# Kernel optimization log

Measured on AMD Instinct MI355X. Metric: run time of the kernel, lower is better.

## Reference

```python
import jax, jax.numpy as jnp
import numpy as np

EMBED = 768
NHEADS = 12
HEAD_DIM = EMBED // NHEADS
LA_HEADS = 16
MLP_HID = EMBED * 4
EPS = 1e-5


def setup_inputs() -> dict:
    key = jax.random.key(0)
    ks = jax.random.split(key, 16)
    s = lambda fan_in: 1.0 / np.sqrt(fan_in)
    inp = {
        "x": jax.random.normal(ks[0], (64, 197, EMBED), dtype=jnp.float32),
        "norm1_g": jnp.ones((EMBED,), jnp.float32),
        "norm1_b": jnp.zeros((EMBED,), jnp.float32),
        "qkv_w": jax.random.normal(ks[1], (3 * EMBED, EMBED), jnp.float32) * s(EMBED),
        "qkv_b": jnp.zeros((3 * EMBED,), jnp.float32),
        "proj_w": jax.random.normal(ks[2], (EMBED, EMBED), jnp.float32) * s(EMBED),
        "proj_b": jnp.zeros((EMBED,), jnp.float32),
        "norm2_g": jnp.ones((EMBED,), jnp.float32),
        "norm2_b": jnp.zeros((EMBED,), jnp.float32),
        "fc1_w": jax.random.normal(ks[3], (MLP_HID, EMBED), jnp.float32) * s(EMBED),
        "fc1_b": jnp.zeros((MLP_HID,), jnp.float32),
        "fc2_w": jax.random.normal(ks[4], (EMBED, MLP_HID), jnp.float32) * s(MLP_HID),
        "fc2_b": jnp.zeros((EMBED,), jnp.float32),
        # LA params: f1 Conv2d(16,1,1) -> weight [16]; f2 Conv2d(1,16,1) -> weight [16]; v Conv2d(2,1,1) -> weight [2]
        "f1_w": jax.random.normal(ks[5], (LA_HEADS,), jnp.float32) * s(LA_HEADS),
        "f1_b": jnp.zeros((1,), jnp.float32),
        "f2_w": jax.random.normal(ks[6], (LA_HEADS,), jnp.float32),
        "f2_b": jnp.zeros((LA_HEADS,), jnp.float32),
        "v_w": jax.random.normal(ks[7], (2,), jnp.float32) * s(2),
        "v_b": jnp.zeros((1,), jnp.float32),
    }
    return inp


def _layernorm(x, g, b):
    mu = x.mean(-1, keepdims=True)
    var = jnp.mean((x - mu) ** 2, -1, keepdims=True)
    return (x - mu) * jax.lax.rsqrt(var + EPS) * g + b


def _la(x, f1_w, f1_b, f2_w, f2_b, v_w, v_b):
    # x: [B, C=768, 14, 14]; 16 channel groups of 48, pooled over 7x7 grid of 2x2 patches
    B, C, H, W = x.shape
    g = C // LA_HEADS
    xr = x.reshape(B, LA_HEADS, g, 7, 2, 7, 2)
    means = xr.mean(axis=(2, 4, 6))            # [B,16,7,7]
    maxs = xr.max(axis=(2, 4, 6))              # [B,16,7,7]

    def channel_mlp(t):  # f2(relu(f1(t))), 1x1 convs across the 16 "head" channels
        h = jnp.einsum('bchw,c->bhw', t, f1_w) + f1_b[0]
        h = jax.nn.relu(h)
        return h[:, None, :, :] * f2_w[None, :, None, None] + f2_b[None, :, None, None]

    m = channel_mlp(means)
    mx = channel_mlp(maxs)
    fusion = v_w[0] * m + v_w[1] * mx + v_b[0]   # [B,16,7,7]
    # bilinear upsample 7x7 -> 14x14, align_corners=False (half-pixel centers)
    fusion = jax.image.resize(fusion, (B, LA_HEADS, 14, 14), method='bilinear')
    gate = jax.nn.sigmoid(fusion)                # [B,16,14,14]
    out = x.reshape(B, LA_HEADS, g, H, W) * gate[:, :, None, :, :]
    return out.reshape(B, C, H, W) + x


def _attn(x, qkv_w, qkv_b, proj_w, proj_b):
    B, N, D = x.shape
    qkv = x @ qkv_w.T + qkv_b
    qkv = qkv.reshape(B, N, 3, NHEADS, HEAD_DIM).transpose(2, 0, 3, 1, 4)
    q, k, v = qkv[0], qkv[1], qkv[2]             # [B,H,N,hd]
    scores = jnp.einsum('bhnd,bhmd->bhnm', q, k) * (HEAD_DIM ** -0.5)
    a = jax.nn.softmax(scores, axis=-1)
    o = jnp.einsum('bhnm,bhmd->bhnd', a, v)
    o = o.transpose(0, 2, 1, 3).reshape(B, N, D)
    return o @ proj_w.T + proj_b


def reference(x, norm1_g, norm1_b, qkv_w, qkv_b, proj_w, proj_b,
              norm2_g, norm2_b, fc1_w, fc1_b, fc2_w, fc2_b,
              f1_w, f1_b, f2_w, f2_b, v_w, v_b):
    B, N, C = x.shape
    cls_tok = x[:, :1, :]                        # [B,1,C]
    spatial = x[:, 1:, :]                        # [B,196,C]
    H = W = 14
    x_la = spatial.reshape(B, H, W, C).transpose(0, 3, 1, 2)   # [B,C,14,14]
    x_la = _la(x_la, f1_w, f1_b, f2_w, f2_b, v_w, v_b)
    x_la = x_la.reshape(B, C, H * W).transpose(0, 2, 1)        # [B,196,C]
    x_cat = jnp.concatenate([cls_tok, x_la], axis=1)           # [B,197,C]
    x = x + _attn(_layernorm(x_cat, norm1_g, norm1_b), qkv_w, qkv_b, proj_w, proj_b)
    h = _layernorm(x, norm2_g, norm2_b)
    h = jax.nn.gelu(h @ fc1_w.T + fc1_b, approximate=False)
    x = x + (h @ fc2_w.T + fc2_b)
    return x
```

## Files before the change

kernel.cpp:

```cpp
#include <hip/hip_runtime.h>
#include <hip/hip_bf16.h>
#include <math.h>

using bf16 = __hip_bfloat16;
using short8 = __attribute__((ext_vector_type(8))) short;
using floatx4 = __attribute__((ext_vector_type(4))) float;

constexpr int B = 64;
constexpr int N = 197;
constexpr int C = 768;
constexpr int NH = 12;
constexpr int HD = 64;
constexpr int HID = 3072;
constexpr int M = B * N;
constexpr int MPAD = 12672;
constexpr int MT = MPAD / 128;
constexpr int MTP = 104;
constexpr float EPS = 1e-5f;

__device__ __forceinline__ float b2f(bf16 v) { return __bfloat162float(v); }
__device__ __forceinline__ bf16 f2b(float v) { return __float2bfloat16(v); }

typedef const __attribute__((address_space(1))) unsigned int* gas1_t;
typedef __attribute__((address_space(3))) unsigned int* las3_t;
__device__ __forceinline__ void load_lds16(const bf16* g, bf16* l) {
  __builtin_amdgcn_global_load_lds((gas1_t)g, (las3_t)l, 16, 0, 0);
}

__global__ void cvt_wf_kernel(const float* __restrict__ src, bf16* __restrict__ dst,
                              int Nc, int K) {
  int i = blockIdx.x * 256 + threadIdx.x;
  int total = Nc * (K >> 3);
  if (i >= total) return;
  int k8 = i % (K >> 3);
  int n  = i / (K >> 3);
  int kc = k8 >> 2, quad = k8 & 3;
  int nb = n >> 7, nn = n & 127, tp = nn >> 4, l = nn & 15;
  int KC = K >> 5;
  size_t di = (((size_t)nb * KC + kc) * 8 + tp) * 512 + quad * 128 + l * 8;
  const float* s = src + (size_t)n * K + k8 * 8;
  #pragma unroll
  for (int e = 0; e < 8; ++e) dst[di + e] = f2b(s[e]);
}

__device__ __forceinline__ float block_sum(float v, float* red) {
  #pragma unroll
  for (int off = 32; off >= 1; off >>= 1) v += __shfl_xor(v, off, 64);
  int w = threadIdx.x >> 6;
  if ((threadIdx.x & 63) == 0) red[w] = v;
  __syncthreads();
  float r = red[0] + red[1] + red[2] + red[3];
  __syncthreads();
  return r;
}

__global__ void la_pool_kernel(const float* __restrict__ x,
                               const float* __restrict__ f1w, const float* __restrict__ f1bias,
                               const float* __restrict__ f2w, const float* __restrict__ f2bias,
                               const float* __restrict__ vw,  const float* __restrict__ vbias,
                               float* __restrict__ fusion7) {
  int blk = blockIdx.x;
  int b = blk / 49, p = blk % 49;
  int h7 = p / 7, w7 = p % 7;
  int tid = threadIdx.x;
  int head = tid >> 4;
  int j = tid & 15;

  float sum = 0.f, mx = -3.0e38f;
  #pragma unroll
  for (int a = 0; a < 2; ++a) {
    #pragma unroll
    for (int bb = 0; bb < 2; ++bb) {
      int tok = 1 + (2 * h7 + a) * 14 + (2 * w7 + bb);
      const float* row = x + ((size_t)b * N + tok) * C + head * 48;
      #pragma unroll
      for (int s = 0; s < 3; ++s) {
        float v = row[j + 16 * s];
        sum += v;
        mx = fmaxf(mx, v);
      }
    }
  }
  #pragma unroll
  for (int off = 8; off >= 1; off >>= 1) {
    sum += __shfl_xor(sum, off, 64);
    mx = fmaxf(mx, __shfl_xor(mx, off, 64));
  }
  __shared__ float s_mean[16], s_max[16];
  if (j == 0) { s_mean[head] = sum / 192.f; s_max[head] = mx; }
  __syncthreads();
  if (tid < 16) {
    float hm = f1bias[0], hx = hm;
    #pragma unroll
    for (int h = 0; h < 16; ++h) {
      float w = f1w[h];
      hm += s_mean[h] * w;
      hx += s_max[h] * w;
    }
    hm = fmaxf(hm, 0.f);
    hx = fmaxf(hx, 0.f);
    float w2 = f2w[tid], b2v = f2bias[tid];
    float m   = hm * w2 + b2v;
    float mxv = hx * w2 + b2v;
    float fus = vw[0] * m + vw[1] * mxv + vbias[0];
    fusion7[((size_t)b * 16 + tid) * 49 + p] = fus;
  }
}

__global__ void gate_ln1_kernel(const float* __restrict__ x, const float* __restrict__ fusion7,
                                const float* __restrict__ g, const float* __restrict__ beta,
                                bf16* __restrict__ ln1) {
  int blk = blockIdx.x;
  int b = blk / N, n = blk % N;
  int tid = threadIdx.x;
  __shared__ float gates[16];
  __shared__ float red[4];

  if (tid < 16) {
    if (n > 0) {
      int hh = (n - 1) / 14, ww = (n - 1) % 14;
      float ch = fminf(fmaxf(hh * 0.5f - 0.25f, 0.f), 6.f);
      float cw = fminf(fmaxf(ww * 0.5f - 0.25f, 0.f), 6.f);
      int h0 = (int)floorf(ch); int h1 = min(h0 + 1, 6); float fh = ch - (float)h0;
      int w0 = (int)floorf(cw); int w1 = min(w0 + 1, 6); float fw = cw - (float)w0;
      const float* fp = fusion7 + ((size_t)b * 16 + tid) * 49;
      float v00 = fp[h0 * 7 + w0], v01 = fp[h0 * 7 + w1];
      float v10 = fp[h1 * 7 + w0], v11 = fp[h1 * 7 + w1];
      float v = (1.f - fh) * ((1.f - fw) * v00 + fw * v01)
              + fh        * ((1.f - fw) * v10 + fw * v11);
      gates[tid] = 1.f / (1.f + expf(-v));
    } else {
      gates[tid] = 0.f;
    }
  }
  __syncthreads();

  const float* xr = x + ((size_t)b * N + n) * C;
  float v[3];
  #pragma unroll
  for (int s = 0; s < 3; ++s) {
    int c = tid + 256 * s;
    v[s] = xr[c] * (1.f + gates[c / 48]);
  }
  float mu = block_sum(v[0] + v[1] + v[2], red) * (1.f / 768.f);
  float d0 = v[0] - mu, d1 = v[1] - mu, d2 = v[2] - mu;
  float var = block_sum(d0 * d0 + d1 * d1 + d2 * d2, red) * (1.f / 768.f);
  float rs = rsqrtf(var + EPS);
  bf16* orow = ln1 + ((size_t)b * N + n) * C;
  #pragma unroll
  for (int s = 0; s < 3; ++s) {
    int c = tid + 256 * s;
    orow[c] = f2b((v[s] - mu) * rs * g[c] + beta[c]);
  }
}

__global__ void ln_bf16_kernel(const bf16* __restrict__ xin,
                               const float* __restrict__ g, const float* __restrict__ beta,
                               bf16* __restrict__ out) {
  int row = blockIdx.x;
  int tid = threadIdx.x;
  __shared__ float red[4];
  const bf16* xr = xin + (size_t)row * C;
  float v[3];
  #pragma unroll
  for (int s = 0; s < 3; ++s) v[s] = b2f(xr[tid + 256 * s]);
  float mu = block_sum(v[0] + v[1] + v[2], red) * (1.f / 768.f);
  float d0 = v[0] - mu, d1 = v[1] - mu, d2 = v[2] - mu;
  float var = block_sum(d0 * d0 + d1 * d1 + d2 * d2, red) * (1.f / 768.f);
  float rs = rsqrtf(var + EPS);
  bf16* orow = out + (size_t)row * C;
  #pragma unroll
  for (int s = 0; s < 3; ++s) {
    int c = tid + 256 * s;
    orow[c] = f2b((v[s] - mu) * rs * g[c] + beta[c]);
  }
}

template <int EPI, int K>
__global__ void __launch_bounds__(256, 3)
gemm128(const bf16* __restrict__ A, const bf16* __restrict__ Wf,
        const float* __restrict__ bias,
        const float* __restrict__ resF, const bf16* __restrict__ resB,
        bf16* __restrict__ outB, float* __restrict__ outF, int Nc) {
  constexpr int KC = K >> 5;
  static_assert(KC % 3 == 0, "KC must be divisible by 3 for the unroll");
  constexpr int CW = (K == 768) ? 6 : 3;
  constexpr int PERCH = 13 * CW;
  int nx = Nc >> 7;
  int g = blockIdx.x;
  int c = g & 7;
  int t = g >> 3;
  int ch = t / PERCH;
  int r  = t % PERCH;
  int j  = r / CW;
  int x  = ch * CW + (r % CW);
  int y  = c + 8 * j;
  if (y >= MT) return;
  int m0 = y * 128;
  int n0 = x * 128;

  __shared__ __align__(16) char smem[49152];
  bf16* sA = (bf16*)smem;
  bf16* sB = (bf16*)(smem + 24576);

  int tid = threadIdx.x;
  int wave = tid >> 6, lane = tid & 63, quad = lane >> 4, l16 = lane & 15;

  int ln16 = lane >> 2, seg = lane & 3;
  int sw = seg ^ ((ln16 >> 1) & 3);
  const bf16* gA = A + (size_t)(m0 + wave * 32 + ln16) * K + sw * 8;

  const bf16* gB = Wf + ((size_t)(n0 >> 7) * KC) * 4096 + (size_t)(wave * 2) * 512 + lane * 8;

  int wm = (wave & 1) * 64, wn = (wave >> 1) * 64;
  int csw = (l16 >> 1) & 3;
  int tp0 = wn >> 4;

  floatx4 acc[4][4] = {};

  bf16* dA0 = sA + (wave * 32) * 32;
  bf16* dB0 = sB + (wave * 2) * 512;

  auto stageTo = [&](const bf16* gAs, const bf16* gBs, int bufOff) {
    load_lds16(gAs, dA0 + bufOff);
    load_lds16(gAs + (size_t)16 * K, dA0 + bufOff + 16 * 32);
    load_lds16(gBs, dB0 + bufOff);
    load_lds16(gBs + 512, dB0 + bufOff + 512);
  };

  stageTo(gA, gB, 0);
  stageTo(gA + 32, gB + 4096, 4096);

  const bf16* gAs = gA + 64;
  const bf16* gBs = gB + 8192;

  const bf16* aRd = sA + (wm + l16) * 32 + (quad ^ csw) * 8;
  const bf16* bRd = sB + tp0 * 512 + lane * 8;

  auto body = [&](int bufOff, int stageBufOff, bool doStage, bool lastIter) {
    if (lastIter) {
      asm volatile("s_waitcnt vmcnt(0) lgkmcnt(0)" ::: "memory");
    } else {
      asm volatile("s_waitcnt vmcnt(4) lgkmcnt(0)" ::: "memory");
    }
    __builtin_amdgcn_s_barrier();
    __builtin_amdgcn_sched_barrier(0);

    short8 bw[4];
    #pragma unroll
    for (int t2 = 0; t2 < 4; ++t2)
      bw[t2] = *reinterpret_cast<const short8*>(bRd + bufOff + t2 * 512);
    short8 af[4];
    #pragma unroll
    for (int s = 0; s < 4; ++s)
      af[s] = *reinterpret_cast<const short8*>(aRd + bufOff + s * 16 * 32);

    if (doStage) {
      stageTo(gAs, gBs, stageBufOff);
      gAs += 32;
      gBs += 4096;
    }

    __builtin_amdgcn_s_setprio(1);
    #pragma unroll
    for (int s = 0; s < 4; ++s)
      #pragma unroll
      for (int t2 = 0; t2 < 4; ++t2)
        acc[s][t2] = __builtin_amdgcn_mfma_f32_16x16x32_bf16(af[s], bw[t2], acc[s][t2], 0, 0, 0);
    __builtin_amdgcn_s_setprio(0);
  };

  for (int kc0 = 0; kc0 < KC; kc0 += 3) {
    bool lastGrp = (kc0 + 3 >= KC);
    body(0,    8192, true,      false);
    body(4096, 0,    !lastGrp,  false);
    body(8192, 4096, !lastGrp,  lastGrp);
  }

  if (!resF && !resB && outB) {
    __syncthreads();
    bf16* sC = (bf16*)smem;
    constexpr int SCS = 136;
    #pragma unroll
    for (int t2 = 0; t2 < 4; ++t2) {
      int col = wn + t2 * 16 + l16;
      float bv = bias[n0 + col];
      #pragma unroll
      for (int s = 0; s < 4; ++s) {
        int rowb = wm + s * 16 + quad * 4;
        #pragma unroll
        for (int r2 = 0; r2 < 4; ++r2) {
          float v = acc[s][t2][r2] + bv;
          if (EPI == 1) v = 0.5f * v * (1.f + erff(v * 0.7071067811865475f));
          sC[(rowb + r2) * SCS + col] = f2b(v);
        }
      }
    }
    __syncthreads();
    int rl = tid >> 4, cl = tid & 15;
    #pragma unroll
    for (int i = 0; i < 8; ++i) {
      int row = i * 16 + rl;
      int gr = m0 + row;
      if (gr < M) {
        short8 vv = *reinterpret_cast<const short8*>(sC + row * SCS + cl * 8);
        *reinterpret_cast<short8*>(outB + (size_t)gr * Nc + n0 + cl * 8) = vv;
      }
    }
  } else {
    #pragma unroll
    for (int t2 = 0; t2 < 4; ++t2) {
      int col = n0 + wn + t2 * 16 + l16;
      float bv = bias[col];
      #pragma unroll
      for (int s = 0; s < 4; ++s) {
        int rowb = m0 + wm + s * 16 + quad * 4;
        #pragma unroll
        for (int r2 = 0; r2 < 4; ++r2) {
          int row = rowb + r2;
          if (row < M) {
            float v = acc[s][t2][r2] + bv;
            if (EPI == 1) v = 0.5f * v * (1.f + erff(v * 0.7071067811865475f));
            size_t idx = (size_t)row * Nc + col;
            if (resF) v += resF[idx];
            if (resB) v += b2f(resB[idx]);
            if (outF) outF[idx] = v;
            if (outB) outB[idx] = f2b(v);
          }
        }
      }
    }
  }
}

__global__ void __launch_bounds__(256, 2)
attn_mfma_kernel(const bf16* __restrict__ qkv, bf16* __restrict__ attn_o) {
  int bh = blockIdx.x;
  int h = bh % NH, b = bh / NH;
  int tid = threadIdx.x;
  int wave = tid >> 6, lane = tid & 63, quad = lane >> 4, l16 = lane & 15;

  __shared__ __align__(16) bf16 sVt[64][232];
  __shared__ __align__(16) bf16 sP[4][16][232];

  const bf16* base = qkv + (size_t)b * N * 2304 + h * 64;

  {
    int d = tid & 63;
    for (int m = tid >> 6; m < 224; m += 4) {
      sVt[d][m] = (m < N) ? base[(size_t)m * 2304 + 1536 + d] : f2b(0.f);
    }
  }
  __syncthreads();

  const float scale = 0.125f;

  for (int qt = wave; qt < 13; qt += 4) {
    int qr = min(qt * 16 + l16, N - 1);
    const bf16* qp = base + (size_t)qr * 2304;
    short8 aq0 = *reinterpret_cast<const short8*>(qp + quad * 8);
    short8 aq1 = *reinterpret_cast<const short8*>(qp + 32 + quad * 8);

    floatx4 s[13];
    short8 bk0c, bk1c;
    {
      int kr = min(l16, N - 1);
      const bf16* kp = base + (size_t)kr * 2304 + 768;
      bk0c = *reinterpret_cast<const short8*>(kp + quad * 8);
      bk1c = *reinterpret_cast<const short8*>(kp + 32 + quad * 8);
    }
    #pragma unroll
    for (int kt = 0; kt < 13; ++kt) {
      short8 bk0n, bk1n;
      if (kt < 12) {
        int kr = min((kt + 1) * 16 + l16, N - 1);
        const bf16* kp = base + (size_t)kr * 2304 + 768;
        bk0n = *reinterpret_cast<const short8*>(kp + quad * 8);
        bk1n = *reinterpret_cast<const short8*>(kp + 32 + quad * 8);
      }
      floatx4 acc = floatx4{0.f, 0.f, 0.f, 0.f};
      acc = __builtin_amdgcn_mfma_f32_16x16x32_bf16(aq0, bk0c, acc, 0, 0, 0);
      acc = __builtin_amdgcn_mfma_f32_16x16x32_bf16(aq1, bk1c, acc, 0, 0, 0);
      s[kt] = acc;
      if (kt < 12) { bk0c = bk0n; bk1c = bk1n; }
    }

    bool cv[13];
    #pragma unroll
    for (int kt = 0; kt < 13; ++kt) cv[kt] = (kt * 16 + l16) < N;

    float mx[4] = {-3.0e38f, -3.0e38f, -3.0e38f, -3.0e38f};
    #pragma unroll
    for (int kt = 0; kt < 13; ++kt) {
      #pragma unroll
      for (int r = 0; r < 4; ++r) {
        float sv = s[kt][r] * scale;
        s[kt][r] = sv;
        if (cv[kt]) mx[r] = fmaxf(mx[r], sv);
      }
    }
    #pragma unroll
    for (int off = 8; off >= 1; off >>= 1) {
      #pragma unroll
      for (int r = 0; r < 4; ++r) mx[r] = fmaxf(mx[r], __shfl_xor(mx[r], off, 64));
    }
    float sum[4] = {0.f, 0.f, 0.f, 0.f};
    #pragma unroll
    for (int kt = 0; kt < 13; ++kt) {
      #pragma unroll
      for (int r = 0; r < 4; ++r) {
        float e = cv[kt] ? __expf(s[kt][r] - mx[r]) : 0.f;
        s[kt][r] = e;
        sum[r] += e;
      }
    }
    #pragma unroll
    for (int off = 8; off >= 1; off >>= 1) {
      #pragma unroll
      for (int r = 0; r < 4; ++r) sum[r] += __shfl_xor(sum[r], off, 64);
    }
    float inv[4];
    #pragma unroll
    for (int r = 0; r < 4; ++r) inv[r] = 1.f / sum[r];

    #pragma unroll
    for (int kt = 0; kt < 13; ++kt) {
      #pragma unroll
      for (int r = 0; r < 4; ++r)
        sP[wave][quad * 4 + r][kt * 16 + l16] = f2b(s[kt][r]);
    }
    #pragma unroll
    for (int r = 0; r < 4; ++r)
      sP[wave][quad * 4 + r][208 + l16] = f2b(0.f);

    floatx4 o[4] = {floatx4{0,0,0,0}, floatx4{0,0,0,0}, floatx4{0,0,0,0}, floatx4{0,0,0,0}};
    #pragma unroll
    for (int c = 0; c < 7; ++c) {
      short8 ap = *reinterpret_cast<const short8*>(&sP[wave][l16][c * 32 + quad * 8]);
      #pragma unroll
      for (int t = 0; t < 4; ++t) {
        short8 bv = *reinterpret_cast<const short8*>(&sVt[t * 16 + l16][c * 32 + quad * 8]);
        o[t] = __builtin_amdgcn_mfma_f32_16x16x32_bf16(ap, bv, o[t], 0, 0, 0);
      }
    }

    asm volatile("s_waitcnt lgkmcnt(0)" ::: "memory");
    bf16* sO = &sP[wave][0][0];
    constexpr int SOS = 72;
    #pragma unroll
    for (int t = 0; t < 4; ++t) {
      #pragma unroll
      for (int r = 0; r < 4; ++r)
        sO[(quad * 4 + r) * SOS + t * 16 + l16] = f2b(o[t][r] * inv[r]);
    }
    asm volatile("s_waitcnt lgkmcnt(0)" ::: "memory");
    int orow = lane >> 3, ocol = (lane & 7) * 8;
    #pragma unroll
    for (int i = 0; i < 2; ++i) {
      int row = i * 8 + orow;
      int qrow = qt * 16 + row;
      if (qrow < N) {
        short8 vv = *reinterpret_cast<const short8*>(sO + row * SOS + ocol);
        *reinterpret_cast<short8*>(attn_o + ((size_t)b * N + qrow) * C + h * 64 + ocol) = vv;
      }
    }
    asm volatile("s_waitcnt lgkmcnt(0)" ::: "memory");
  }
}

extern "C" void kernel_launch(void* const* d_in, const int* in_sizes, int n_in,
                              void* d_out, int out_size, void* d_ws, size_t ws_size,
                              hipStream_t stream) {
  (void)in_sizes; (void)n_in; (void)out_size; (void)ws_size;
  const float* x       = (const float*)d_in[0];
  const float* norm1_g = (const float*)d_in[1];
  const float* norm1_b = (const float*)d_in[2];
  const float* qkv_w   = (const float*)d_in[3];
  const float* qkv_b   = (const float*)d_in[4];
  const float* proj_w  = (const float*)d_in[5];
  const float* proj_b  = (const float*)d_in[6];
  const float* norm2_g = (const float*)d_in[7];
  const float* norm2_b = (const float*)d_in[8];
  const float* fc1_w   = (const float*)d_in[9];
  const float* fc1_b   = (const float*)d_in[10];
  const float* fc2_w   = (const float*)d_in[11];
  const float* fc2_b   = (const float*)d_in[12];
  const float* f1_w    = (const float*)d_in[13];
  const float* f1_b    = (const float*)d_in[14];
  const float* f2_w    = (const float*)d_in[15];
  const float* f2_b    = (const float*)d_in[16];
  const float* v_w     = (const float*)d_in[17];
  const float* v_b     = (const float*)d_in[18];
  float* out = (float*)d_out;

  char* ws = (char*)d_ws;
  float* fusion7 = (float*)(ws + 0);
  bf16*  qkv_wf  = (bf16*)(ws + 262144);
  bf16*  proj_wf = (bf16*)(ws + 3801088);
  bf16*  fc1_wf  = (bf16*)(ws + 4980736);
  bf16*  fc2_wf  = (bf16*)(ws + 9699328);
  bf16*  ln1     = (bf16*)(ws + 14417920);
  bf16*  attn_o  = ln1;
  bf16*  ln2     = ln1;
  bf16*  qkvb    = (bf16*)(ws + 33882112);
  bf16*  hbuf    = qkvb;
  bf16*  x2b     = (bf16*)(ws + 111738880);

  cvt_wf_kernel<<<(2304 * 96 + 255) / 256, 256, 0, stream>>>(qkv_w, qkv_wf, 2304, 768);
  cvt_wf_kernel<<<(768 * 96 + 255) / 256, 256, 0, stream>>>(proj_w, proj_wf, 768, 768);
  cvt_wf_kernel<<<(3072 * 96 + 255) / 256, 256, 0, stream>>>(fc1_w, fc1_wf, 3072, 768);
  cvt_wf_kernel<<<(768 * 384 + 255) / 256, 256, 0, stream>>>(fc2_w, fc2_wf, 768, 3072);

  la_pool_kernel<<<B * 49, 256, 0, stream>>>(x, f1_w, f1_b, f2_w, f2_b, v_w, v_b, fusion7);
  gate_ln1_kernel<<<B * N, 256, 0, stream>>>(x, fusion7, norm1_g, norm1_b, ln1);
  gemm128<0, 768><<<(2304 / 128) * MTP, 256, 0, stream>>>(
      ln1, qkv_wf, qkv_b, nullptr, nullptr, qkvb, nullptr, 2304);
  attn_mfma_kernel<<<B * NH, 256, 0, stream>>>(qkvb, attn_o);
  gemm128<0, 768><<<(768 / 128) * MTP, 256, 0, stream>>>(
      attn_o, proj_wf, proj_b, x, nullptr, x2b, nullptr, 768);
  ln_bf16_kernel<<<M, 256, 0, stream>>>(x2b, norm2_g, norm2_b, ln2);
  gemm128<1, 768><<<(HID / 128) * MTP, 256, 0, stream>>>(
      ln2, fc1_wf, fc1_b, nullptr, nullptr, hbuf, nullptr, HID);
  gemm128<0, 3072><<<(768 / 128) * MTP, 256, 0, stream>>>(
      hbuf, fc2_wf, fc2_b, nullptr, x2b, nullptr, out, 768);
}
```

Baseline: 541.5 us.

## Load GEMM weight fragments directly to registers, halving LDS to raise occupancy

The B (weight) operand is no longer staged through shared memory. Each wave loads its pre-swizzled weight fragments straight from global memory into double-buffered registers, one k-step ahead. Shared memory drops to the A buffers only, so launch bounds rise to 4 blocks per CU. The epilogue now writes the output tile through LDS in two 64-row halves to fit the smaller buffer. The cost is more VGPR pressure, and each wave pulling its own weights from global/L2 gives up reuse across waves.

```diff
diff --git a/kernel.cpp b/kernel.cpp
--- a/kernel.cpp
+++ b/kernel.cpp
@@ -177,13 +177,13 @@
 }
 
 template <int EPI, int K>
-__global__ void __launch_bounds__(256, 3)
+__global__ void __launch_bounds__(256, 4)
 gemm128(const bf16* __restrict__ A, const bf16* __restrict__ Wf,
         const float* __restrict__ bias,
         const float* __restrict__ resF, const bf16* __restrict__ resB,
         bf16* __restrict__ outB, float* __restrict__ outF, int Nc) {
   constexpr int KC = K >> 5;
-  static_assert(KC % 3 == 0, "KC must be divisible by 3 for the unroll");
+  static_assert(KC % 6 == 0, "KC must be divisible by 6 for the unroll");
   constexpr int CW = (K == 768) ? 6 : 3;
   constexpr int PERCH = 13 * CW;
   int nx = Nc >> 7;
@@ -199,9 +199,8 @@
   int m0 = y * 128;
   int n0 = x * 128;
 
-  __shared__ __align__(16) char smem[49152];
+  __shared__ __align__(16) char smem[24576];
   bf16* sA = (bf16*)smem;
-  bf16* sB = (bf16*)(smem + 24576);
 
   int tid = threadIdx.x;
   int wave = tid >> 6, lane = tid & 63, quad = lane >> 4, l16 = lane & 15;
@@ -210,55 +209,57 @@
   int sw = seg ^ ((ln16 >> 1) & 3);
   const bf16* gA = A + (size_t)(m0 + wave * 32 + ln16) * K + sw * 8;
 
-  const bf16* gB = Wf + ((size_t)(n0 >> 7) * KC) * 4096 + (size_t)(wave * 2) * 512 + lane * 8;
-
   int wm = (wave & 1) * 64, wn = (wave >> 1) * 64;
   int csw = (l16 >> 1) & 3;
   int tp0 = wn >> 4;
 
+  const bf16* gBf = Wf + ((size_t)(n0 >> 7) * KC) * 4096 + (size_t)tp0 * 512 + lane * 8;
+
   floatx4 acc[4][4] = {};
 
   bf16* dA0 = sA + (wave * 32) * 32;
-  bf16* dB0 = sB + (wave * 2) * 512;
-
-  auto stageTo = [&](const bf16* gAs, const bf16* gBs, int bufOff) {
+
+  auto stageA = [&](const bf16* gAs, int bufOff) {
     load_lds16(gAs, dA0 + bufOff);
     load_lds16(gAs + (size_t)16 * K, dA0 + bufOff + 16 * 32);
-    load_lds16(gBs, dB0 + bufOff);
-    load_lds16(gBs + 512, dB0 + bufOff + 512);
   };
 
-  stageTo(gA, gB, 0);
-  stageTo(gA + 32, gB + 4096, 4096);
+  short8 bA[4], bB[4];
+  stageA(gA, 0);
+  #pragma unroll
+  for (int t2 = 0; t2 < 4; ++t2)
+    bA[t2] = *reinterpret_cast<const short8*>(gBf + t2 * 512);
+  stageA(gA + 32, 4096);
 
   const bf16* gAs = gA + 64;
-  const bf16* gBs = gB + 8192;
+  const bf16* gBs = gBf + 4096;
 
   const bf16* aRd = sA + (wm + l16) * 32 + (quad ^ csw) * 8;
-  const bf16* bRd = sB + tp0 * 512 + lane * 8;
-
-  auto body = [&](int bufOff, int stageBufOff, bool doStage, bool lastIter) {
+
+  auto body = [&](int bufOff, int stageBufOff, short8 (&rd)[4], short8 (&ld)[4],
+                  bool doStageA, bool doLoadB, bool lastIter) {
     if (lastIter) {
-      asm volatile("s_waitcnt vmcnt(0) lgkmcnt(0)" ::: "memory");
+      asm volatile("s_waitcnt vmcnt(4) lgkmcnt(0)" ::: "memory");
     } else {
-      asm volatile("s_waitcnt vmcnt(4) lgkmcnt(0)" ::: "memory");
+      asm volatile("s_waitcnt vmcnt(6) lgkmcnt(0)" ::: "memory");
     }
     __builtin_amdgcn_s_barrier();
     __builtin_amdgcn_sched_barrier(0);
 
-    short8 bw[4];
-    #pragma unroll
-    for (int t2 = 0; t2 < 4; ++t2)
-      bw[t2] = *reinterpret_cast<const short8*>(bRd + bufOff + t2 * 512);
     short8 af[4];
     #pragma unroll
     for (int s = 0; s < 4; ++s)
       af[s] = *reinterpret_cast<const short8*>(aRd + bufOff + s * 16 * 32);
 
-    if (doStage) {
-      stageTo(gAs, gBs, stageBufOff);
+    if (doLoadB) {
+      #pragma unroll
+      for (int t2 = 0; t2 < 4; ++t2)
+        ld[t2] = *reinterpret_cast<const short8*>(gBs + t2 * 512);
+      gBs += 4096;
+    }
+    if (doStageA) {
+      stageA(gAs, stageBufOff);
       gAs += 32;
-      gBs += 4096;
     }
 
     __builtin_amdgcn_s_setprio(1);
@@ -266,45 +267,53 @@
     for (int s = 0; s < 4; ++s)
       #pragma unroll
       for (int t2 = 0; t2 < 4; ++t2)
-        acc[s][t2] = __builtin_amdgcn_mfma_f32_16x16x32_bf16(af[s], bw[t2], acc[s][t2], 0, 0, 0);
+        acc[s][t2] = __builtin_amdgcn_mfma_f32_16x16x32_bf16(af[s], rd[t2], acc[s][t2], 0, 0, 0);
     __builtin_amdgcn_s_setprio(0);
   };
 
-  for (int kc0 = 0; kc0 < KC; kc0 += 3) {
-    bool lastGrp = (kc0 + 3 >= KC);
-    body(0,    8192, true,      false);
-    body(4096, 0,    !lastGrp,  false);
-    body(8192, 4096, !lastGrp,  lastGrp);
+  for (int kc0 = 0; kc0 < KC; kc0 += 6) {
+    bool last = (kc0 + 6 >= KC);
+    body(0,    8192, bA, bB, true,  true,  false);
+    body(4096, 0,    bB, bA, true,  true,  false);
+    body(8192, 4096, bA, bB, true,  true,  false);
+    body(0,    8192, bB, bA, true,  true,  false);
+    body(4096, 0,    bA, bB, !last, true,  false);
+    body(8192, 4096, bB, bA, !last, !last, last);
   }
 
   if (!resF && !resB && outB) {
-    __syncthreads();
     bf16* sC = (bf16*)smem;
     constexpr int SCS = 136;
     #pragma unroll
-    for (int t2 = 0; t2 < 4; ++t2) {
-      int col = wn + t2 * 16 + l16;
-      float bv = bias[n0 + col];
-      #pragma unroll
-      for (int s = 0; s < 4; ++s) {
-        int rowb = wm + s * 16 + quad * 4;
+    for (int half = 0; half < 2; ++half) {
+      __syncthreads();
+      if (wm == half * 64) {
         #pragma unroll
-        for (int r2 = 0; r2 < 4; ++r2) {
-          float v = acc[s][t2][r2] + bv;
-          if (EPI == 1) v = 0.5f * v * (1.f + erff(v * 0.7071067811865475f));
-          sC[(rowb + r2) * SCS + col] = f2b(v);
+        for (int t2 = 0; t2 < 4; ++t2) {
+          int col = wn + t2 * 16 + l16;
+          float bv = bias[n0 + col];
+          #pragma unroll
+          for (int s = 0; s < 4; ++s) {
+            int rowb = s * 16 + quad * 4;
+            #pragma unroll
+            for (int r2 = 0; r2 < 4; ++r2) {
+              float v = acc[s][t2][r2] + bv;
+              if (EPI == 1) v = 0.5f * v * (1.f + erff(v * 0.7071067811865475f));
+              sC[(rowb + r2) * SCS + col] = f2b(v);
+            }
+          }
         }
       }
-    }
-    __syncthreads();
-    int rl = tid >> 4, cl = tid & 15;
-    #pragma unroll
-    for (int i = 0; i < 8; ++i) {
-      int row = i * 16 + rl;
-      int gr = m0 + row;
-      if (gr < M) {
-        short8 vv = *reinterpret_cast<const short8*>(sC + row * SCS + cl * 8);
-        *reinterpret_cast<short8*>(outB + (size_t)gr * Nc + n0 + cl * 8) = vv;
+      __syncthreads();
+      int rl = tid >> 4, cl = tid & 15;
+      #pragma unroll
+      for (int i = 0; i < 4; ++i) {
+        int row = i * 16 + rl;
+        int gr = m0 + half * 64 + row;
+        if (gr < M) {
+          short8 vv = *reinterpret_cast<const short8*>(sC + row * SCS + cl * 8);
+          *reinterpret_cast<short8*>(outB + (size_t)gr * Nc + n0 + cl * 8) = vv;
+        }
       }
     }
   } else {
```

New measurement: 683.3 us. 26.2% more time.
